# Kernel optimization log

Hardware: AMD Instinct MI355X
Metric: run time of the kernel (lower is better)

## Reference

```python
import jax, jax.numpy as jnp
import numpy as np

B, N, D, H = 32, 1024, 512, 8

def setup_inputs() -> dict:
    key = jax.random.key(0)
    ks = jax.random.split(key, 11)
    std = D ** (-0.5)
    inp = {
        'k': jax.random.normal(ks[0], (B, N, D), jnp.float32),
        'v': jax.random.normal(ks[1], (B, N, D), jnp.float32),
        'q': jax.random.normal(ks[2], (B, N, D), jnp.float32),
        # per-head Linear weights, torch layout (out, in), stacked over heads
        'Wk': jax.random.normal(ks[3], (H, D, D), jnp.float32) * std,
        'bk': jax.random.uniform(ks[4], (H, D), jnp.float32, -std, std),
        'Wv': jax.random.normal(ks[5], (H, D, D), jnp.float32) * std,
        'bv': jax.random.uniform(ks[6], (H, D), jnp.float32, -std, std),
        'Wq': jax.random.normal(ks[7], (H, D, D), jnp.float32) * std,
        'bq': jax.random.uniform(ks[8], (H, D), jnp.float32, -std, std),
        # output projection: (hidden, n_heads*hidden)
        'Wo': jax.random.normal(ks[9], (D, H * D), jnp.float32) * (H * D) ** (-0.5),
        'bo': jax.random.uniform(ks[10], (D,), jnp.float32, -(H * D) ** (-0.5), (H * D) ** (-0.5)),
    }
    return inp

def reference(k, v, q, Wk, bk, Wv, bv, Wq, bq, Wo, bo):
    # Batched per-head projections (torch Linear: y = x @ W.T + b)
    kh = jnp.einsum('bnd,hed->bhne', k, Wk) + bk[:, None, :]  # [B,H,N,D]
    vh = jnp.einsum('bnd,hed->bhne', v, Wv) + bv[:, None, :]
    qh = jnp.einsum('bnd,hed->bhne', q, Wq) + bq[:, None, :]
    scale = jnp.asarray(qh.shape[-1] ** 0.5, qh.dtype)
    scores = jnp.einsum('bhjd,bhid->bhij', kh, qh) / scale      # [B,H,Nq,Nk]
    w = jax.nn.softmax(scores, axis=-1)
    out = jnp.einsum('bhij,bhjd->bhid', w, vh)                  # [B,H,Nq,D]
    # torch stacks heads on last dim then flattens: out[..., d, h] -> d*H + h
    cat = out.transpose(0, 2, 3, 1).reshape(out.shape[0], out.shape[2], -1)  # [B,Nq,D*H]
    rep = cat @ Wo.T + bo                                        # [B,Nq,D]
    return rep
```

## Files before the change

kernel.cpp:

```cpp
#include <hip/hip_runtime.h>
#include <hip/hip_bf16.h>
#include <cstdint>
#include <type_traits>

constexpr int B_SZ = 32;
constexpr int N_SZ = 1024;
constexpr int D_SZ = 512;
constexpr int H_SZ = 8;
constexpr int HD   = H_SZ * D_SZ;

typedef __attribute__((ext_vector_type(8))) short short8;
typedef __attribute__((ext_vector_type(4))) float floatx4;
typedef unsigned short u16;
typedef unsigned int   u32;

static __device__ __forceinline__ u16 f2bf(float f) {
    union { float f; unsigned int i; } c; c.f = f;
    unsigned int x = c.i;
    unsigned int r = x + 0x7FFFu + ((x >> 16) & 1u);
    return (u16)(r >> 16);
}

static __device__ __forceinline__ u32 cvt_pk_bf16(float a, float b) {
    u32 r;
    asm("v_cvt_pk_bf16_f32 %0, %1, %2" : "=v"(r) : "v"(a), "v"(b));
    return r;
}

__global__ void cvt_kernel(const float* __restrict__ src, u16* __restrict__ dst) {
    int idx = (blockIdx.x * 256 + threadIdx.x) * 4;
    float4 v = *(const float4*)(src + idx);
    ushort4 o;
    o.x = f2bf(v.x); o.y = f2bf(v.y); o.z = f2bf(v.z); o.w = f2bf(v.w);
    *(ushort4*)(dst + idx) = o;
}

__global__ void woperm_kernel(const float* __restrict__ Wo, u16* __restrict__ Wp) {
    int idx = blockIdx.x * 256 + threadIdx.x;
    int e = idx >> 12;
    int c = idx & 4095;
    int d  = c & 511;
    int hh = c >> 9;
    Wp[idx] = f2bf(Wo[((size_t)e << 12) + d * H_SZ + hh]);
}

template<typename AT, int OM>
__global__ __launch_bounds__(256, 2)
void gemm_bt(const AT* __restrict__ A, const u16* __restrict__ W,
             const float* __restrict__ bias, void* __restrict__ Cout,
             int M, int Nc, int K)
{
    __shared__ u16 Alds[128 * 40];
    __shared__ u16 Blds[128 * 40];
    const int tid  = threadIdx.x;
    const int lane = tid & 63;
    const int wave = tid >> 6;
    const int wm = wave >> 1, wn = wave & 1;
    const int m16 = lane & 15, quad = lane >> 4;
    const size_t tm0 = (size_t)blockIdx.x * 128;
    const size_t tn0 = (size_t)blockIdx.y * 128;

    floatx4 acc[4][4];
#pragma unroll
    for (int i = 0; i < 4; i++)
#pragma unroll
        for (int j = 0; j < 4; j++) acc[i][j] = (floatx4){0.f, 0.f, 0.f, 0.f};

    const int srow  = tid >> 1;
    const int skoff = (tid & 1) * 16;
    const AT*  ag = A + (tm0 + srow) * (size_t)K + skoff;
    const u16* bg = W + (tn0 + srow) * (size_t)K + skoff;

    for (int k0 = 0; k0 < K; k0 += 32) {
        short8 a0, a1;
        if constexpr (std::is_same_v<AT, float>) {
            float4 f0 = *(const float4*)(ag + k0);
            float4 f1 = *(const float4*)(ag + k0 + 4);
            float4 f2 = *(const float4*)(ag + k0 + 8);
            float4 f3 = *(const float4*)(ag + k0 + 12);
            a0 = (short8){(short)f2bf(f0.x), (short)f2bf(f0.y), (short)f2bf(f0.z), (short)f2bf(f0.w),
                          (short)f2bf(f1.x), (short)f2bf(f1.y), (short)f2bf(f1.z), (short)f2bf(f1.w)};
            a1 = (short8){(short)f2bf(f2.x), (short)f2bf(f2.y), (short)f2bf(f2.z), (short)f2bf(f2.w),
                          (short)f2bf(f3.x), (short)f2bf(f3.y), (short)f2bf(f3.z), (short)f2bf(f3.w)};
        } else {
            a0 = *(const short8*)(ag + k0);
            a1 = *(const short8*)(ag + k0 + 8);
        }
        short8 b0 = *(const short8*)(bg + k0);
        short8 b1 = *(const short8*)(bg + k0 + 8);
        __syncthreads();
        *(short8*)&Alds[srow * 40 + skoff]     = a0;
        *(short8*)&Alds[srow * 40 + skoff + 8] = a1;
        *(short8*)&Blds[srow * 40 + skoff]     = b0;
        *(short8*)&Blds[srow * 40 + skoff + 8] = b1;
        __syncthreads();
        short8 af[4], bf[4];
#pragma unroll
        for (int t = 0; t < 4; t++) {
            af[t] = *(const short8*)&Alds[(wm * 64 + t * 16 + m16) * 40 + quad * 8];
            bf[t] = *(const short8*)&Blds[(wn * 64 + t * 16 + m16) * 40 + quad * 8];
        }
#pragma unroll
        for (int i = 0; i < 4; i++)
#pragma unroll
            for (int j = 0; j < 4; j++)
                acc[i][j] = __builtin_amdgcn_mfma_f32_16x16x32_bf16(af[i], bf[j], acc[i][j], 0, 0, 0);
    }

#pragma unroll
    for (int j = 0; j < 4; j++) {
        int col = (int)tn0 + wn * 64 + j * 16 + m16;
        float bsv = bias[col];
#pragma unroll
        for (int i = 0; i < 4; i++) {
            size_t row = tm0 + wm * 64 + i * 16 + quad * 4;
            if constexpr (OM == 2) {
                int cloc = (int)(row >> 10);
                int n0   = (int)(row & 1023);
                ushort4 pk;
                pk.x = f2bf(acc[i][j][0] + bsv);
                pk.y = f2bf(acc[i][j][1] + bsv);
                pk.z = f2bf(acc[i][j][2] + bsv);
                pk.w = f2bf(acc[i][j][3] + bsv);
                u16* vtp = (u16*)Cout;
                *(ushort4*)&vtp[((size_t)cloc * HD + col) * N_SZ + n0] = pk;
            } else {
#pragma unroll
                for (int r = 0; r < 4; r++) {
                    if constexpr (OM == 1)
                        ((float*)Cout)[(row + r) * (size_t)Nc + col] = acc[i][j][r] + bsv;
                    else
                        ((u16*)Cout)[(row + r) * (size_t)Nc + col] = f2bf(acc[i][j][r] + bsv);
                }
            }
        }
    }
}

__global__ __launch_bounds__(256, 2)
void attn_kernel(const u16* __restrict__ qh, const u16* __restrict__ kh,
                 const u16* __restrict__ vt, u16* __restrict__ ao)
{
    __shared__ u16 Klds[32 * 512];
    __shared__ u16 Vtlds[512 * 32];
    u16*   Pov    = Klds;
    float* alphaF = (float*)&Klds[2560];
    float* lF     = (float*)&Klds[2688];
    u32*   flagp  = (u32*)&Klds[2816];

    const int tid  = threadIdx.x;
    const int lane = tid & 63;
    const int wave = tid >> 6;
    const int m16  = lane & 15;
    const int quad = lane >> 4;

    const int orig = blockIdx.x + ((int)blockIdx.y << 4) + ((int)blockIdx.z << 7);
    const int cpx  = ((int)gridDim.z << 7) >> 3;
    const int swz  = (orig & 7) * cpx + (orig >> 3);
    const int qt = swz & 15;
    const int h  = (swz >> 4) & 7;
    const int bb = swz >> 7;

    const int kxor = m16 & 7;
    const int qx8  = (quad ^ (kxor & 3)) * 8;
    const int kx32 = (kxor & 4) * 8;
    const u16* kaddrE = &Klds[m16 * 512 + qx8 + kx32];
    const u16* kaddrO = &Klds[m16 * 512 + qx8 - kx32];
    const int vx8 = (quad ^ (m16 & 3) ^ ((m16 >> 2) & 3)) * 8;
    const u16* vaddr = &Vtlds[m16 * 32 + vx8];
    const int ebase = wave * 16 + (lane >> 2);
    const int cw8   = ((lane & 3) ^ ((lane >> 2) & 3) ^ ((lane >> 4) & 3)) * 8;

    const int qrow = qt * 64 + wave * 16 + m16;
    const u16* qptr = qh + ((size_t)(bb * N_SZ + qrow)) * HD + h * D_SZ + quad * 8;
    short8 qfrag[16];
#pragma unroll
    for (int kk = 0; kk < 16; kk++)
        qfrag[kk] = *(const short8*)(qptr + kk * 32);

    floatx4 acc[8][4];
#pragma unroll
    for (int j = 0; j < 8; j++)
#pragma unroll
        for (int qc = 0; qc < 4; qc++) acc[j][qc] = (floatx4){0.f, 0.f, 0.f, 0.f};

    float mrow = -3.0e38f, lrow = 0.f;

    const float scale = 0.04419417382415922f;
    const u16* kbase  = kh + ((size_t)(bb * N_SZ)) * HD + h * D_SZ;
    const u16* vtbase = vt + ((size_t)bb * HD + h * D_SZ) * N_SZ;

    short8 kreg[8];
#pragma unroll
    for (int i = 0; i < 8; i++) {
        int row = i * 4 + wave;
        kreg[i] = *(const short8*)(kbase + (size_t)row * HD + lane * 8);
    }

    for (int kt = 0; kt < 32; kt++) {
        __syncthreads();
#pragma unroll
        for (int i = 0; i < 8; i++) {
            int row = i * 4 + wave;
            int cp  = lane ^ (row & 7);
            *(short8*)&Klds[row * 512 + cp * 8] = kreg[i];
        }
        __syncthreads();

        short8 vreg[8];
#pragma unroll
        for (int i = 0; i < 8; i++) {
            int e = i * 64 + ebase;
            vreg[i] = *(const short8*)(vtbase + (size_t)e * N_SZ + kt * 32 + (lane & 3) * 8);
        }

        floatx4 s0a = (floatx4){0.f,0.f,0.f,0.f}, s0b = s0a, s1a = s0a, s1b = s0a;
        __builtin_amdgcn_s_setprio(1);
#pragma unroll
        for (int kk = 0; kk < 16; kk++) {
            const u16* p = (kk & 1) ? kaddrO : kaddrE;
            short8 kb0 = *(const short8*)(p + kk * 32);
            short8 kb1 = *(const short8*)(p + kk * 32 + 8192);
            if (kk & 1) {
                s0b = __builtin_amdgcn_mfma_f32_16x16x32_bf16(kb0, qfrag[kk], s0b, 0, 0, 0);
                s1b = __builtin_amdgcn_mfma_f32_16x16x32_bf16(kb1, qfrag[kk], s1b, 0, 0, 0);
            } else {
                s0a = __builtin_amdgcn_mfma_f32_16x16x32_bf16(kb0, qfrag[kk], s0a, 0, 0, 0);
                s1a = __builtin_amdgcn_mfma_f32_16x16x32_bf16(kb1, qfrag[kk], s1a, 0, 0, 0);
            }
        }
        __builtin_amdgcn_s_setprio(0);
        floatx4 s0 = s0a + s0b;
        floatx4 s1 = s1a + s1b;

        float a[8];
#pragma unroll
        for (int r = 0; r < 4; r++) { a[r] = s0[r] * scale; a[4 + r] = s1[r] * scale; }
        float pm = fmaxf(fmaxf(fmaxf(a[0], a[1]), fmaxf(a[2], a[3])),
                         fmaxf(fmaxf(a[4], a[5]), fmaxf(a[6], a[7])));
        pm = fmaxf(pm, __shfl_xor(pm, 16, 64));
        pm = fmaxf(pm, __shfl_xor(pm, 32, 64));
        float alpha = 1.0f;
        u32 wflag = 0u;
        if (__any(pm > mrow + 8.0f)) {
            float mnew = fmaxf(mrow, pm);
            alpha = __expf(mrow - mnew);
            mrow = mnew;
            wflag = 1u;
        }
        float p[8];
        float ps = 0.f;
#pragma unroll
        for (int i = 0; i < 8; i++) { p[i] = __expf(a[i] - mrow); ps += p[i]; }
        ps += __shfl_xor(ps, 16, 64);
        ps += __shfl_xor(ps, 32, 64);
        lrow = lrow * alpha + ps;

        u32 w0 = cvt_pk_bf16(p[0], p[1]);
        u32 w1 = cvt_pk_bf16(p[2], p[3]);
        u32 w2 = cvt_pk_bf16(p[4], p[5]);
        u32 w3 = cvt_pk_bf16(p[6], p[7]);

        int ktn = (kt < 31) ? (kt + 1) : kt;
#pragma unroll
        for (int i = 0; i < 8; i++) {
            int row = i * 4 + wave;
            kreg[i] = *(const short8*)(kbase + (size_t)(ktn * 32 + row) * HD + lane * 8);
        }

        __syncthreads();

#pragma unroll
        for (int i = 0; i < 8; i++) {
            int e = i * 64 + ebase;
            *(short8*)&Vtlds[e * 32 + cw8] = vreg[i];
        }
        {
            int q40 = (wave * 16 + m16) * 40;
            uint2 lo; lo.x = w0; lo.y = w1;
            uint2 hi; hi.x = w2; hi.y = w3;
            *(uint2*)&Pov[q40 + quad * 4]      = lo;
            *(uint2*)&Pov[q40 + 16 + quad * 4] = hi;
        }
        if (quad == 0) alphaF[wave * 16 + m16] = alpha;
        if (lane == 0) flagp[wave] = wflag;
        __syncthreads();

        u32 f = flagp[0] | flagp[1] | flagp[2] | flagp[3];
        if (f) {
#pragma unroll
            for (int qc = 0; qc < 4; qc++) {
#pragma unroll
                for (int r = 0; r < 4; r++) {
                    float av = alphaF[qc * 16 + quad * 4 + r];
#pragma unroll
                    for (int j = 0; j < 8; j++) acc[j][qc][r] *= av;
                }
            }
        }

        short8 pf[4];
#pragma unroll
        for (int qc = 0; qc < 4; qc++)
            pf[qc] = *(const short8*)&Pov[(qc * 16 + m16) * 40 + quad * 8];
        __builtin_amdgcn_s_setprio(1);
#pragma unroll
        for (int j = 0; j < 8; j++) {
            short8 vf = *(const short8*)(vaddr + (wave * 8 + j) * 512);
#pragma unroll
            for (int qc = 0; qc < 4; qc++)
                acc[j][qc] = __builtin_amdgcn_mfma_f32_16x16x32_bf16(pf[qc], vf, acc[j][qc], 0, 0, 0);
        }
        __builtin_amdgcn_s_setprio(0);
    }

    if (quad == 0) lF[wave * 16 + m16] = lrow;
    __syncthreads();
#pragma unroll
    for (int qc = 0; qc < 4; qc++) {
#pragma unroll
        for (int r = 0; r < 4; r++) {
            int row = qt * 64 + qc * 16 + quad * 4 + r;
            float invl = 1.0f / lF[qc * 16 + quad * 4 + r];
            size_t obase = ((size_t)(bb * N_SZ + row)) * HD + h * D_SZ + wave * 128;
#pragma unroll
            for (int j = 0; j < 8; j++)
                ao[obase + j * 16 + m16] = f2bf(acc[j][qc][r] * invl);
        }
    }
}

extern "C" void kernel_launch(void* const* d_in, const int* in_sizes, int n_in,
                              void* d_out, int out_size, void* d_ws, size_t ws_size,
                              hipStream_t stream)
{
    const float* kin = (const float*)d_in[0];
    const float* vin = (const float*)d_in[1];
    const float* qin = (const float*)d_in[2];
    const float* Wk  = (const float*)d_in[3];
    const float* bk  = (const float*)d_in[4];
    const float* Wv  = (const float*)d_in[5];
    const float* bv  = (const float*)d_in[6];
    const float* Wq  = (const float*)d_in[7];
    const float* bq  = (const float*)d_in[8];
    const float* Wo  = (const float*)d_in[9];
    const float* bo  = (const float*)d_in[10];
    float* out = (float*)d_out;

    u16* ws = (u16*)d_ws;
    const size_t wEl      = (size_t)H_SZ * D_SZ * D_SZ;
    const size_t permEl   = (size_t)D_SZ * HD;
    const size_t perBatch = (size_t)N_SZ * HD;
    const size_t fixedEl  = 3 * wEl + permEl;
    long long availEl = (long long)(ws_size / 2) - (long long)fixedEl;
    int C = 1;
    if (availEl > 0) {
        long long c = availEl / (long long)(4 * perBatch);
        C = (int)(c < 1 ? 1 : (c > B_SZ ? B_SZ : c));
    }

    u16* wqb = ws;
    u16* wkb = wqb + wEl;
    u16* wvb = wkb + wEl;
    u16* wop = wvb + wEl;
    u16* qh  = wop + permEl;
    u16* khb = qh  + (size_t)C * perBatch;
    u16* vtb = khb + (size_t)C * perBatch;
    u16* ao  = vtb + (size_t)C * perBatch;

    const int cvtBlocks = (int)(wEl / 1024);
    cvt_kernel<<<cvtBlocks, 256, 0, stream>>>(Wq, wqb);
    cvt_kernel<<<cvtBlocks, 256, 0, stream>>>(Wk, wkb);
    cvt_kernel<<<cvtBlocks, 256, 0, stream>>>(Wv, wvb);
    woperm_kernel<<<(int)(permEl / 256), 256, 0, stream>>>(Wo, wop);

    for (int b0 = 0; b0 < B_SZ; b0 += C) {
        int Cc = (B_SZ - b0 < C) ? (B_SZ - b0) : C;
        int M = Cc * N_SZ;
        dim3 gp(M / 128, HD / 128);
        gemm_bt<float, 0><<<gp, 256, 0, stream>>>(qin + (size_t)b0 * N_SZ * D_SZ, wqb, bq, qh,  M, HD, D_SZ);
        gemm_bt<float, 0><<<gp, 256, 0, stream>>>(kin + (size_t)b0 * N_SZ * D_SZ, wkb, bk, khb, M, HD, D_SZ);
        gemm_bt<float, 2><<<gp, 256, 0, stream>>>(vin + (size_t)b0 * N_SZ * D_SZ, wvb, bv, vtb, M, HD, D_SZ);
        attn_kernel<<<dim3(N_SZ / 64, H_SZ, Cc), 256, 0, stream>>>(qh, khb, vtb, ao);
        gemm_bt<u16, 1><<<dim3(M / 128, D_SZ / 128), 256, 0, stream>>>(ao, wop, bo,
                                                                       out + (size_t)b0 * N_SZ * D_SZ, M, D_SZ, HD);
    }
}
```

Baseline: 2.965 ms.

## Double-buffer GEMM tiles with direct global-to-LDS loads and pre-convert inputs

The projection GEMM now loads bf16 tiles straight into LDS with global_load_lds and double-buffers them, so the next K-slice is fetched while MFMAs run on the current one. It also drops one barrier per step and remaps workgroups in a grouped swizzle for better L2 reuse. To support this, the fp32 q/k/v inputs are first converted to bf16 in separate kernels, which adds extra passes and workspace in exchange for a simpler, overlapped GEMM inner loop. The unpadded 32-wide LDS rows may cause bank conflicts on fragment reads.

```diff
diff --git a/kernel.cpp b/kernel.cpp
--- a/kernel.cpp
+++ b/kernel.cpp
@@ -25,6 +25,12 @@
     u32 r;
     asm("v_cvt_pk_bf16_f32 %0, %1, %2" : "=v"(r) : "v"(a), "v"(b));
     return r;
+}
+
+static __device__ __forceinline__ void ld2lds16(const u16* g, u16* l) {
+    __builtin_amdgcn_global_load_lds(
+        (const __attribute__((address_space(1))) void*)g,
+        (__attribute__((address_space(3))) void*)l, 16, 0, 0);
 }
 
 __global__ void cvt_kernel(const float* __restrict__ src, u16* __restrict__ dst) {
@@ -44,21 +50,28 @@
     Wp[idx] = f2bf(Wo[((size_t)e << 12) + d * H_SZ + hh]);
 }
 
-template<typename AT, int OM>
+template<int OM>
 __global__ __launch_bounds__(256, 2)
-void gemm_bt(const AT* __restrict__ A, const u16* __restrict__ W,
+void gemm_bt(const u16* __restrict__ A, const u16* __restrict__ W,
              const float* __restrict__ bias, void* __restrict__ Cout,
              int M, int Nc, int K)
 {
-    __shared__ u16 Alds[128 * 40];
-    __shared__ u16 Blds[128 * 40];
+    __shared__ u16 Alds[2][128 * 32];
+    __shared__ u16 Blds[2][128 * 32];
     const int tid  = threadIdx.x;
     const int lane = tid & 63;
     const int wave = tid >> 6;
     const int wm = wave >> 1, wn = wave & 1;
     const int m16 = lane & 15, quad = lane >> 4;
-    const size_t tm0 = (size_t)blockIdx.x * 128;
-    const size_t tn0 = (size_t)blockIdx.y * 128;
+
+    const int nbx = gridDim.x;
+    const int nwg = nbx * (int)gridDim.y;
+    const int wg  = (int)blockIdx.x + (int)blockIdx.y * nbx;
+    const int swz = (wg & 7) * (nwg >> 3) + (wg >> 3);
+    const int bx  = swz % nbx;
+    const int by  = swz / nbx;
+    const size_t tm0 = (size_t)bx * 128;
+    const size_t tn0 = (size_t)by * 128;
 
     floatx4 acc[4][4];
 #pragma unroll
@@ -66,39 +79,37 @@
 #pragma unroll
         for (int j = 0; j < 4; j++) acc[i][j] = (floatx4){0.f, 0.f, 0.f, 0.f};
 
-    const int srow  = tid >> 1;
-    const int skoff = (tid & 1) * 16;
-    const AT*  ag = A + (tm0 + srow) * (size_t)K + skoff;
-    const u16* bg = W + (tn0 + srow) * (size_t)K + skoff;
-
-    for (int k0 = 0; k0 < K; k0 += 32) {
-        short8 a0, a1;
-        if constexpr (std::is_same_v<AT, float>) {
-            float4 f0 = *(const float4*)(ag + k0);
-            float4 f1 = *(const float4*)(ag + k0 + 4);
-            float4 f2 = *(const float4*)(ag + k0 + 8);
-            float4 f3 = *(const float4*)(ag + k0 + 12);
-            a0 = (short8){(short)f2bf(f0.x), (short)f2bf(f0.y), (short)f2bf(f0.z), (short)f2bf(f0.w),
-                          (short)f2bf(f1.x), (short)f2bf(f1.y), (short)f2bf(f1.z), (short)f2bf(f1.w)};
-            a1 = (short8){(short)f2bf(f2.x), (short)f2bf(f2.y), (short)f2bf(f2.z), (short)f2bf(f2.w),
-                          (short)f2bf(f3.x), (short)f2bf(f3.y), (short)f2bf(f3.z), (short)f2bf(f3.w)};
-        } else {
-            a0 = *(const short8*)(ag + k0);
-            a1 = *(const short8*)(ag + k0 + 8);
-        }
-        short8 b0 = *(const short8*)(bg + k0);
-        short8 b1 = *(const short8*)(bg + k0 + 8);
+    const int srow = lane >> 2;
+    const int scol = (lane & 3) * 8;
+    const u16* ag0 = A + (tm0 + wave * 32 + srow) * (size_t)K + scol;
+    const u16* ag1 = ag0 + (size_t)16 * K;
+    const u16* bg0 = W + (tn0 + wave * 32 + srow) * (size_t)K + scol;
+    const u16* bg1 = bg0 + (size_t)16 * K;
+
+    const int nT = K >> 5;
+
+#define STAGE(t, buf)                                            \
+    do {                                                         \
+        size_t ko = (size_t)(t) * 32;                            \
+        u16* al = &Alds[(buf)][wave * 1024];                     \
+        u16* bl = &Blds[(buf)][wave * 1024];                     \
+        ld2lds16(ag0 + ko, al);                                  \
+        ld2lds16(ag1 + ko, al + 512);                            \
+        ld2lds16(bg0 + ko, bl);                                  \
+        ld2lds16(bg1 + ko, bl + 512);                            \
+    } while (0)
+
+    STAGE(0, 0);
+    for (int t = 0; t < nT; ++t) {
         __syncthreads();
-        *(short8*)&Alds[srow * 40 + skoff]     = a0;
-        *(short8*)&Alds[srow * 40 + skoff + 8] = a1;
-        *(short8*)&Blds[srow * 40 + skoff]     = b0;
-        *(short8*)&Blds[srow * 40 + skoff + 8] = b1;
-        __syncthreads();
+        if (t + 1 < nT) STAGE(t + 1, (t + 1) & 1);
+        const u16* Ab = Alds[t & 1];
+        const u16* Bb = Blds[t & 1];
         short8 af[4], bf[4];
 #pragma unroll
-        for (int t = 0; t < 4; t++) {
-            af[t] = *(const short8*)&Alds[(wm * 64 + t * 16 + m16) * 40 + quad * 8];
-            bf[t] = *(const short8*)&Blds[(wn * 64 + t * 16 + m16) * 40 + quad * 8];
+        for (int i = 0; i < 4; i++) {
+            af[i] = *(const short8*)&Ab[(wm * 64 + i * 16 + m16) * 32 + quad * 8];
+            bf[i] = *(const short8*)&Bb[(wn * 64 + i * 16 + m16) * 32 + quad * 8];
         }
 #pragma unroll
         for (int i = 0; i < 4; i++)
@@ -106,6 +117,7 @@
             for (int j = 0; j < 4; j++)
                 acc[i][j] = __builtin_amdgcn_mfma_f32_16x16x32_bf16(af[i], bf[j], acc[i][j], 0, 0, 0);
     }
+#undef STAGE
 
 #pragma unroll
     for (int j = 0; j < 4; j++) {
@@ -350,12 +362,14 @@
     u16* ws = (u16*)d_ws;
     const size_t wEl      = (size_t)H_SZ * D_SZ * D_SZ;
     const size_t permEl   = (size_t)D_SZ * HD;
+    const size_t inEl     = (size_t)N_SZ * D_SZ;
     const size_t perBatch = (size_t)N_SZ * HD;
     const size_t fixedEl  = 3 * wEl + permEl;
+    const size_t perB     = 4 * perBatch + 3 * inEl;
     long long availEl = (long long)(ws_size / 2) - (long long)fixedEl;
     int C = 1;
     if (availEl > 0) {
-        long long c = availEl / (long long)(4 * perBatch);
+        long long c = availEl / (long long)perB;
         C = (int)(c < 1 ? 1 : (c > B_SZ ? B_SZ : c));
     }
 
@@ -363,7 +377,10 @@
     u16* wkb = wqb + wEl;
     u16* wvb = wkb + wEl;
     u16* wop = wvb + wEl;
-    u16* qh  = wop + permEl;
+    u16* qcb = wop + permEl;
+    u16* kcb = qcb + (size_t)C * inEl;
+    u16* vcb = kcb + (size_t)C * inEl;
+    u16* qh  = vcb + (size_t)C * inEl;
     u16* khb = qh  + (size_t)C * perBatch;
     u16* vtb = khb + (size_t)C * perBatch;
     u16* ao  = vtb + (size_t)C * perBatch;
@@ -377,12 +394,16 @@
     for (int b0 = 0; b0 < B_SZ; b0 += C) {
         int Cc = (B_SZ - b0 < C) ? (B_SZ - b0) : C;
         int M = Cc * N_SZ;
+        int cvB = (int)((size_t)Cc * inEl / 1024);
+        cvt_kernel<<<cvB, 256, 0, stream>>>(qin + (size_t)b0 * inEl, qcb);
+        cvt_kernel<<<cvB, 256, 0, stream>>>(kin + (size_t)b0 * inEl, kcb);
+        cvt_kernel<<<cvB, 256, 0, stream>>>(vin + (size_t)b0 * inEl, vcb);
         dim3 gp(M / 128, HD / 128);
-        gemm_bt<float, 0><<<gp, 256, 0, stream>>>(qin + (size_t)b0 * N_SZ * D_SZ, wqb, bq, qh,  M, HD, D_SZ);
-        gemm_bt<float, 0><<<gp, 256, 0, stream>>>(kin + (size_t)b0 * N_SZ * D_SZ, wkb, bk, khb, M, HD, D_SZ);
-        gemm_bt<float, 2><<<gp, 256, 0, stream>>>(vin + (size_t)b0 * N_SZ * D_SZ, wvb, bv, vtb, M, HD, D_SZ);
+        gemm_bt<0><<<gp, 256, 0, stream>>>(qcb, wqb, bq, qh,  M, HD, D_SZ);
+        gemm_bt<0><<<gp, 256, 0, stream>>>(kcb, wkb, bk, khb, M, HD, D_SZ);
+        gemm_bt<2><<<gp, 256, 0, stream>>>(vcb, wvb, bv, vtb, M, HD, D_SZ);
         attn_kernel<<<dim3(N_SZ / 64, H_SZ, Cc), 256, 0, stream>>>(qh, khb, vtb, ao);
-        gemm_bt<u16, 1><<<dim3(M / 128, D_SZ / 128), 256, 0, stream>>>(ao, wop, bo,
-                                                                       out + (size_t)b0 * N_SZ * D_SZ, M, D_SZ, HD);
-    }
-}
+        gemm_bt<1><<<dim3(M / 128, D_SZ / 128), 256, 0, stream>>>(ao, wop, bo,
+                                                                  out + (size_t)b0 * N_SZ * D_SZ, M, D_SZ, HD);
+    }
+}
```

New measurement: 3.113 ms. 5.0% more time.
